# Kernel tuning notes

Hardware: AMD Instinct MI355X
Metric: run time of the kernel (lower is better)

## Reference

```python
import jax, jax.numpy as jnp
import numpy as np

N_NODES = 50000
N_EDGES = 800000
IN_FEAT = 128
HEADS = 8
HEAD_DIM = 16  # out_feat // num_heads = 128 // 8
NEG_SLOPE = 0.2


def setup_inputs() -> dict:
    key = jax.random.key(0)
    ks = jax.random.split(key, 8)
    g = 1.0 / np.sqrt(IN_FEAT)
    return {
        "x": jax.random.normal(ks[0], (N_NODES, IN_FEAT), jnp.float32),
        "efeat": jax.random.normal(ks[1], (N_EDGES, IN_FEAT), jnp.float32),
        "src": jax.random.randint(ks[2], (N_EDGES,), 0, N_NODES),
        "dst": jax.random.randint(ks[3], (N_EDGES,), 0, N_NODES),
        "W_src": jax.random.normal(ks[4], (HEADS * HEAD_DIM, IN_FEAT), jnp.float32) * g,
        "b_src": jnp.zeros((HEADS * HEAD_DIM,), jnp.float32),
        "W_dst": jax.random.normal(ks[5], (HEADS * HEAD_DIM, IN_FEAT), jnp.float32) * g,
        "b_dst": jnp.zeros((HEADS * HEAD_DIM,), jnp.float32),
        "W_edge": jax.random.normal(ks[6], (HEADS * HEAD_DIM, IN_FEAT), jnp.float32) * g,
        "attn": jax.random.normal(ks[7], (HEADS, HEAD_DIM), jnp.float32) * (1.0 / np.sqrt(HEAD_DIM)),
    }


def reference(x, efeat, src, dst, W_src, b_src, W_dst, b_dst, W_edge, attn):
    H, D = HEADS, HEAD_DIM
    # node/edge projections: [N,H,D] / [E,H,D]
    feat_src = (x @ W_src.T + b_src).reshape(-1, H, D)
    feat_dst = (x @ W_dst.T + b_dst).reshape(-1, H, D)
    feat_edge = (efeat @ W_edge.T).reshape(-1, H, D)

    # per-edge GATv2 score: LeakyReLU(src + dst + edge) . attn  -> [E,H]
    fs = feat_src[src]                                    # gather [E,H,D]
    tmp = fs + feat_dst[dst] + feat_edge
    e = jnp.where(tmp >= 0, tmp, NEG_SLOPE * tmp)
    score = jnp.einsum('ehd,hd->eh', e, attn)

    # edge softmax normalized per destination node
    m = jax.ops.segment_max(score, dst, num_segments=N_NODES)     # [N,H]
    ex = jnp.exp(score - jax.lax.stop_gradient(m)[dst])
    z = jax.ops.segment_sum(ex, dst, num_segments=N_NODES)        # [N,H]
    a = ex / z[dst]                                               # [E,H]

    # weighted scatter-sum of (src + edge) messages
    msg = (fs + feat_edge) * a[:, :, None]                        # [E,H,D]
    h = jax.ops.segment_sum(msg, dst, num_segments=N_NODES)       # [N,H,D]

    # res_fc is None since in_feat == H*D; activation = relu
    h = jax.nn.relu(h)
    return h.reshape(N_NODES, H * D)
```

## Files before the change

### kernel.cpp

```cpp
#include <hip/hip_runtime.h>
#include <hip/hip_bf16.h>

#define NNODES 50000
#define NEDGES 800000
#define NEG_SLOPE 0.2f
#define N_PAD 50176

typedef float f32x4 __attribute__((ext_vector_type(4)));
typedef float f32x2 __attribute__((ext_vector_type(2)));
typedef __bf16 bf16x8 __attribute__((ext_vector_type(8)));
typedef __bf16 bf16x4 __attribute__((ext_vector_type(4)));
typedef __bf16 bf16x2 __attribute__((ext_vector_type(2)));

__global__ __launch_bounds__(256) void convert_hist(
    const float* __restrict__ W0, const float* __restrict__ W1,
    const float* __restrict__ W2, __bf16* __restrict__ out,
    const int* __restrict__ dst, int* __restrict__ deg, int* __restrict__ arr)
{
  int b = blockIdx.x;
  if (b < 48) {
    int m = b >> 4;
    const float* W = (m == 0) ? W0 : ((m == 1) ? W1 : W2);
    __bf16* o = out + m * 16384;
    int i = (b & 15) * 1024 + threadIdx.x * 4;
    int r = i >> 7, cx = i & 127;
    f32x4 v = *(const f32x4*)(W + i);
    int kb = cx >> 3, ko = cx & 7;
    int off = r * 128 + ((kb ^ (r & 15)) << 3) + ko;
    bf16x4 pk = { (__bf16)v.x, (__bf16)v.y, (__bf16)v.z, (__bf16)v.w };
    *(bf16x4*)(o + off) = pk;
  } else {
    int e = (b - 48) * 256 + threadIdx.x;
    arr[e] = atomicAdd(&deg[dst[e]], 1);
  }
}

template<int OUT_BF16, int HAS_BIAS, int SCATTER>
__device__ __forceinline__ void gemm_body(
    int tile, const float* __restrict__ A, const __bf16* __restrict__ Wsw,
    const float* __restrict__ bias, const int* __restrict__ rank,
    void* __restrict__ outp, int M, __bf16* sS)
{
  const int t = threadIdx.x;
  const int m0 = tile * 128;

  #pragma unroll
  for (int it = 0; it < 8; ++it) {
    int lin = it * 2048 + t * 8;
    *(bf16x8*)(sS + lin) = *(const bf16x8*)(Wsw + lin);
  }

  const int w = t >> 6, lane = t & 63;
  const int rsel = lane & 15, quad = lane >> 4;

  bf16x8 af[4][2];
  #pragma unroll
  for (int mi = 0; mi < 2; ++mi) {
    int gr = m0 + w * 32 + mi * 16 + rsel;
    const float* p = A + (size_t)gr * 128 + (quad << 3);
    bool ok = gr < M;
    f32x4 r0[4], r1[4];
    #pragma unroll
    for (int kk = 0; kk < 4; ++kk) {
      f32x4 z4 = {0.f, 0.f, 0.f, 0.f};
      r0[kk] = ok ? *(const f32x4*)(p + kk * 32)     : z4;
      r1[kk] = ok ? *(const f32x4*)(p + kk * 32 + 4) : z4;
    }
    #pragma unroll
    for (int kk = 0; kk < 4; ++kk)
      af[kk][mi] = (bf16x8){ (__bf16)r0[kk].x, (__bf16)r0[kk].y, (__bf16)r0[kk].z, (__bf16)r0[kk].w,
                             (__bf16)r1[kk].x, (__bf16)r1[kk].y, (__bf16)r1[kk].z, (__bf16)r1[kk].w };
  }

  f32x4 acc[2][8];
  f32x4 zero = {0.f, 0.f, 0.f, 0.f};
  #pragma unroll
  for (int mi = 0; mi < 2; ++mi)
    #pragma unroll
    for (int ni = 0; ni < 8; ++ni) acc[mi][ni] = zero;

  __syncthreads();

  #pragma unroll
  for (int kk = 0; kk < 4; ++kk) {
    int kb0 = kk * 4 + quad;
    bf16x8 bfr[8];
    #pragma unroll
    for (int ni = 0; ni < 8; ++ni) {
      int r = ni * 16 + rsel;
      bfr[ni] = *(const bf16x8*)(sS + r * 128 + ((kb0 ^ (r & 15)) << 3));
    }
    #pragma unroll
    for (int mi = 0; mi < 2; ++mi)
      #pragma unroll
      for (int ni = 0; ni < 8; ++ni)
        acc[mi][ni] = __builtin_amdgcn_mfma_f32_16x16x32_bf16(af[kk][mi], bfr[ni], acc[mi][ni], 0, 0, 0);
  }

  if (OUT_BF16 && SCATTER) {
    __syncthreads();
    #pragma unroll
    for (int mi = 0; mi < 2; ++mi)
      #pragma unroll
      for (int ni = 0; ni < 8; ++ni)
        #pragma unroll
        for (int r4 = 0; r4 < 4; ++r4) {
          float v = acc[mi][ni][r4];
          float vx = __shfl_xor(v, 1);
          if (!(rsel & 1)) {
            int trow = w * 32 + mi * 16 + quad * 4 + r4;
            bf16x2 pkv = { (__bf16)v, (__bf16)vx };
            *(bf16x2*)(sS + trow * 136 + ni * 16 + rsel) = pkv;
          }
        }
    __syncthreads();
    int tr = t >> 1, h = t & 1;
    int grow = m0 + tr;
    if (grow < M) {
      int orw = rank[grow];
      const __bf16* sp = sS + tr * 136 + h * 64;
      __bf16* dp = (__bf16*)outp + (size_t)orw * 128 + h * 64;
      #pragma unroll
      for (int i = 0; i < 8; ++i)
        *(bf16x8*)(dp + i * 8) = *(const bf16x8*)(sp + i * 8);
    }
  } else {
    #pragma unroll
    for (int mi = 0; mi < 2; ++mi)
      #pragma unroll
      for (int ni = 0; ni < 8; ++ni)
        #pragma unroll
        for (int r4 = 0; r4 < 4; ++r4) {
          int grow = m0 + w * 32 + mi * 16 + quad * 4 + r4;
          int col = ni * 16 + rsel;
          if (grow < M) {
            float v = acc[mi][ni][r4];
            if (HAS_BIAS) v += bias[col];
            ((float*)outp)[(size_t)grow * 128 + col] = v;
          }
        }
  }
}

__global__ __launch_bounds__(256, 4) void proj_all(
    const float* __restrict__ x, const float* __restrict__ efeat,
    const __bf16* __restrict__ wsw, const float* __restrict__ b_src,
    const float* __restrict__ b_dst, const int* __restrict__ rank,
    float* __restrict__ feat_src, float* __restrict__ feat_dst,
    __bf16* __restrict__ fe)
{
  __shared__ __bf16 sS[128 * 136];
  int b = blockIdx.x;
  if (b < 6250)
    gemm_body<1,0,1>(b, efeat, wsw + 32768, nullptr, rank, fe, NEDGES, sS);
  else if (b < 6641)
    gemm_body<0,1,0>(b - 6250, x, wsw, b_src, nullptr, feat_src, NNODES, sS);
  else
    gemm_body<0,1,0>(b - 6641, x, wsw + 16384, b_dst, nullptr, feat_dst, NNODES, sS);
}

__global__ void scan_local(const int* __restrict__ deg, int* __restrict__ scanned,
                           int* __restrict__ bsum){
  __shared__ int s[1024];
  int t = threadIdx.x, i = blockIdx.x * 1024 + t;
  int v = deg[i];
  s[t] = v; __syncthreads();
  #pragma unroll
  for (int off = 1; off < 1024; off <<= 1){
    int x = (t >= off) ? s[t - off] : 0;
    __syncthreads();
    s[t] += x;
    __syncthreads();
  }
  scanned[i] = s[t] - v;
  if (t == 1023) bsum[blockIdx.x] = s[t];
}

__global__ void scan_add(const int* __restrict__ scanned, const int* __restrict__ bsum,
                         int* __restrict__ row_start){
  __shared__ int sbase;
  int b = blockIdx.x, t = threadIdx.x;
  if (t == 0){
    int lim = b >> 2, acc = 0;
    for (int j = 0; j < lim; ++j) acc += bsum[j];
    sbase = acc;
  }
  __syncthreads();
  int i = b * 256 + t;
  if (i < N_PAD) row_start[i] = scanned[i] + sbase;
}

__global__ void scatter_kernel(const int* __restrict__ dst, const int* __restrict__ src,
                               const int* __restrict__ row_start, int* __restrict__ rank,
                               int* __restrict__ src_perm){
  int e = blockIdx.x * 256 + threadIdx.x;
  int pos = row_start[dst[e]] + rank[e];
  rank[e] = pos;
  src_perm[pos] = src[e];
}

__global__ __launch_bounds__(256) void aggregate_fused(
    const int* __restrict__ row_start, const int* __restrict__ deg,
    const int* __restrict__ src_perm, const float* __restrict__ fs,
    const float* __restrict__ fd, const __bf16* __restrict__ fe,
    const float* __restrict__ attn, float* __restrict__ out)
{
  int wv = threadIdx.x >> 6, lane = threadIdx.x & 63;
  int n = blockIdx.x * 4 + wv;
  int row = row_start[n], dg = deg[n];
  int c = lane << 1;
  f32x2 fdv = *(const f32x2*)(fd + (size_t)n * 128 + c);
  f32x2 atv = *(const f32x2*)(attn + c);
  float acc0 = 0.f, acc1 = 0.f, zs = 0.f;
  const __bf16* fep = fe + (size_t)row * 128 + c;

  #define EDGE_BODY(FV, EV)                                            \
    {                                                                  \
      float v0 = (FV).x + (float)(EV).x;                               \
      float v1 = (FV).y + (float)(EV).y;                               \
      float t0 = v0 + fdv.x; t0 = t0 >= 0.f ? t0 : NEG_SLOPE * t0;     \
      float t1 = v1 + fdv.y; t1 = t1 >= 0.f ? t1 : NEG_SLOPE * t1;     \
      float p = t0 * atv.x + t1 * atv.y;                               \
      p += __shfl_xor(p, 1);                                           \
      p += __shfl_xor(p, 2);                                           \
      p += __shfl_xor(p, 4);                                           \
      float ex = __expf(p);                                            \
      acc0 += ex * v0; acc1 += ex * v1; zs += ex;                      \
    }

  for (int base = 0; base < dg; base += 64){
    int cnt = min(64, dg - base);
    int si = 0;
    if (lane < cnt) si = src_perm[row + base + lane];
    int j = 0;
    for (; j + 4 <= cnt; j += 4){
      int s0 = __shfl(si, j,     64);
      int s1 = __shfl(si, j + 1, 64);
      int s2 = __shfl(si, j + 2, 64);
      int s3 = __shfl(si, j + 3, 64);
      f32x2 f0 = *(const f32x2*)(fs + (size_t)s0 * 128 + c);
      f32x2 f1 = *(const f32x2*)(fs + (size_t)s1 * 128 + c);
      f32x2 f2 = *(const f32x2*)(fs + (size_t)s2 * 128 + c);
      f32x2 f3 = *(const f32x2*)(fs + (size_t)s3 * 128 + c);
      bf16x2 e0 = *(const bf16x2*)(fep + (size_t)(base + j)     * 128);
      bf16x2 e1 = *(const bf16x2*)(fep + (size_t)(base + j + 1) * 128);
      bf16x2 e2 = *(const bf16x2*)(fep + (size_t)(base + j + 2) * 128);
      bf16x2 e3 = *(const bf16x2*)(fep + (size_t)(base + j + 3) * 128);
      EDGE_BODY(f0, e0)
      EDGE_BODY(f1, e1)
      EDGE_BODY(f2, e2)
      EDGE_BODY(f3, e3)
    }
    for (; j < cnt; ++j){
      int s0 = __shfl(si, j, 64);
      f32x2 f0 = *(const f32x2*)(fs + (size_t)s0 * 128 + c);
      bf16x2 e0 = *(const bf16x2*)(fep + (size_t)(base + j) * 128);
      EDGE_BODY(f0, e0)
    }
  }
  #undef EDGE_BODY

  float rz = zs > 0.f ? 1.f / zs : 0.f;
  float o0 = acc0 * rz, o1 = acc1 * rz;
  f32x2 ov = { o0 > 0.f ? o0 : 0.f, o1 > 0.f ? o1 : 0.f };
  *(f32x2*)(out + (size_t)n * 128 + c) = ov;
}

extern "C" void kernel_launch(void* const* d_in, const int* in_sizes, int n_in,
                              void* d_out, int out_size, void* d_ws, size_t ws_size,
                              hipStream_t stream)
{
  const float* x      = (const float*)d_in[0];
  const float* efeat  = (const float*)d_in[1];
  const int*   src    = (const int*)d_in[2];
  const int*   dst    = (const int*)d_in[3];
  const float* W_src  = (const float*)d_in[4];
  const float* b_src  = (const float*)d_in[5];
  const float* W_dst  = (const float*)d_in[6];
  const float* b_dst  = (const float*)d_in[7];
  const float* W_edge = (const float*)d_in[8];
  const float* attn   = (const float*)d_in[9];

  char* ws = (char*)d_ws;
  float*  feat_src  = (float*)(ws + 0);
  float*  feat_dst  = (float*)(ws + 25600000);
  __bf16* fe        = (__bf16*)(ws + 51200000);
  int*    src_perm  = (int*)  (ws + 256000000);
  int*    rank      = (int*)  (ws + 259200000);
  int*    row_start = (int*)  (ws + 262400000);
  int*    scanned   = (int*)  (ws + 262801408);
  int*    deg       = (int*)  (ws + 263002112);
  int*    bsum      = (int*)  (ws + 263202816);
  __bf16* wsw       = (__bf16*)(ws + 263203840);

  hipMemsetAsync(deg, 0, 200704, stream);

  convert_hist<<<3173, 256, 0, stream>>>(W_src, W_dst, W_edge, wsw, dst, deg, rank);

  scan_local    <<<49, 1024, 0, stream>>>(deg, scanned, bsum);
  scan_add      <<<196, 256, 0, stream>>>(scanned, bsum, row_start);
  scatter_kernel<<<3125, 256, 0, stream>>>(dst, src, row_start, rank, src_perm);

  proj_all<<<7032, 256, 0, stream>>>(x, efeat, wsw, b_src, b_dst, rank,
                                     feat_src, feat_dst, fe);

  aggregate_fused<<<12500, 256, 0, stream>>>(row_start, deg, src_perm, feat_src,
                                             feat_dst, fe, attn, (float*)d_out);
}
```

Baseline: 770.8 us.

## Move per-edge score and message computation into the edge projection epilogue

The node projection GEMMs are merged into the scan_add kernel launch, and the scatter kernel is removed. The edge GEMM epilogue now gathers the src and dst node features, computes the per-head attention score and its exp, and writes the bf16 message (fs+fe) and the exp values to CSR-sorted positions. Aggregation then becomes a streaming weighted sum over contiguous messages with no random gathers or shuffle reductions. In exchange it writes an extra exp buffer and a bf16 message buffer. Softmax is now computed without subtracting the segment max, which could overflow for large scores.

Result: slower. 909.7 us (+18.0%).

```diff
diff --git a/kernel.cpp b/kernel.cpp
--- a/kernel.cpp
+++ b/kernel.cpp
@@ -35,11 +35,9 @@
   }
 }
 
-template<int OUT_BF16, int HAS_BIAS, int SCATTER>
-__device__ __forceinline__ void gemm_body(
+__device__ __forceinline__ void gemm_node(
     int tile, const float* __restrict__ A, const __bf16* __restrict__ Wsw,
-    const float* __restrict__ bias, const int* __restrict__ rank,
-    void* __restrict__ outp, int M, __bf16* sS)
+    const float* __restrict__ bias, float* __restrict__ outp, int M, __bf16* sS)
 {
   const int t = threadIdx.x;
   const int m0 = tile * 128;
@@ -97,66 +95,17 @@
         acc[mi][ni] = __builtin_amdgcn_mfma_f32_16x16x32_bf16(af[kk][mi], bfr[ni], acc[mi][ni], 0, 0, 0);
   }
 
-  if (OUT_BF16 && SCATTER) {
-    __syncthreads();
-    #pragma unroll
-    for (int mi = 0; mi < 2; ++mi)
-      #pragma unroll
-      for (int ni = 0; ni < 8; ++ni)
-        #pragma unroll
-        for (int r4 = 0; r4 < 4; ++r4) {
-          float v = acc[mi][ni][r4];
-          float vx = __shfl_xor(v, 1);
-          if (!(rsel & 1)) {
-            int trow = w * 32 + mi * 16 + quad * 4 + r4;
-            bf16x2 pkv = { (__bf16)v, (__bf16)vx };
-            *(bf16x2*)(sS + trow * 136 + ni * 16 + rsel) = pkv;
-          }
-        }
-    __syncthreads();
-    int tr = t >> 1, h = t & 1;
-    int grow = m0 + tr;
-    if (grow < M) {
-      int orw = rank[grow];
-      const __bf16* sp = sS + tr * 136 + h * 64;
-      __bf16* dp = (__bf16*)outp + (size_t)orw * 128 + h * 64;
-      #pragma unroll
-      for (int i = 0; i < 8; ++i)
-        *(bf16x8*)(dp + i * 8) = *(const bf16x8*)(sp + i * 8);
-    }
-  } else {
-    #pragma unroll
-    for (int mi = 0; mi < 2; ++mi)
-      #pragma unroll
-      for (int ni = 0; ni < 8; ++ni)
-        #pragma unroll
-        for (int r4 = 0; r4 < 4; ++r4) {
-          int grow = m0 + w * 32 + mi * 16 + quad * 4 + r4;
-          int col = ni * 16 + rsel;
-          if (grow < M) {
-            float v = acc[mi][ni][r4];
-            if (HAS_BIAS) v += bias[col];
-            ((float*)outp)[(size_t)grow * 128 + col] = v;
-          }
-        }
-  }
-}
-
-__global__ __launch_bounds__(256, 4) void proj_all(
-    const float* __restrict__ x, const float* __restrict__ efeat,
-    const __bf16* __restrict__ wsw, const float* __restrict__ b_src,
-    const float* __restrict__ b_dst, const int* __restrict__ rank,
-    float* __restrict__ feat_src, float* __restrict__ feat_dst,
-    __bf16* __restrict__ fe)
-{
-  __shared__ __bf16 sS[128 * 136];
-  int b = blockIdx.x;
-  if (b < 6250)
-    gemm_body<1,0,1>(b, efeat, wsw + 32768, nullptr, rank, fe, NEDGES, sS);
-  else if (b < 6641)
-    gemm_body<0,1,0>(b - 6250, x, wsw, b_src, nullptr, feat_src, NNODES, sS);
-  else
-    gemm_body<0,1,0>(b - 6641, x, wsw + 16384, b_dst, nullptr, feat_dst, NNODES, sS);
+  #pragma unroll
+  for (int mi = 0; mi < 2; ++mi)
+    #pragma unroll
+    for (int ni = 0; ni < 8; ++ni)
+      #pragma unroll
+      for (int r4 = 0; r4 < 4; ++r4) {
+        int grow = m0 + w * 32 + mi * 16 + quad * 4 + r4;
+        int col = ni * 16 + rsel;
+        if (grow < M)
+          outp[(size_t)grow * 128 + col] = acc[mi][ni][r4] + bias[col];
+      }
 }
 
 __global__ void scan_local(const int* __restrict__ deg, int* __restrict__ scanned,
@@ -176,92 +125,188 @@
   if (t == 1023) bsum[blockIdx.x] = s[t];
 }
 
-__global__ void scan_add(const int* __restrict__ scanned, const int* __restrict__ bsum,
-                         int* __restrict__ row_start){
+__global__ __launch_bounds__(256, 4) void scan_nodes(
+    const int* __restrict__ scanned, const int* __restrict__ bsum,
+    int* __restrict__ row_start,
+    const float* __restrict__ x, const __bf16* __restrict__ wsw,
+    const float* __restrict__ b_src, const float* __restrict__ b_dst,
+    float* __restrict__ feat_src, float* __restrict__ feat_dst)
+{
+  __shared__ __bf16 sS[128 * 136];
   __shared__ int sbase;
-  int b = blockIdx.x, t = threadIdx.x;
-  if (t == 0){
-    int lim = b >> 2, acc = 0;
-    for (int j = 0; j < lim; ++j) acc += bsum[j];
-    sbase = acc;
-  }
+  int b = blockIdx.x;
+  if (b < 196) {
+    int t = threadIdx.x;
+    if (t == 0){
+      int lim = b >> 2, a = 0;
+      for (int j = 0; j < lim; ++j) a += bsum[j];
+      sbase = a;
+    }
+    __syncthreads();
+    int i = b * 256 + t;
+    if (i < N_PAD) row_start[i] = scanned[i] + sbase;
+  } else if (b < 587) {
+    gemm_node(b - 196, x, wsw,         b_src, feat_src, NNODES, sS);
+  } else {
+    gemm_node(b - 587, x, wsw + 16384, b_dst, feat_dst, NNODES, sS);
+  }
+}
+
+__global__ __launch_bounds__(256, 4) void proj_edge(
+    const float* __restrict__ efeat, const __bf16* __restrict__ Wsw,
+    const int* __restrict__ src, const int* __restrict__ dst,
+    const int* __restrict__ arr, const int* __restrict__ row_start,
+    const float* __restrict__ fs, const float* __restrict__ fd,
+    const float* __restrict__ attn,
+    __bf16* __restrict__ msg, float* __restrict__ exbuf)
+{
+  __shared__ __bf16 sS[128 * 136];
+  const int t = threadIdx.x;
+  const int m0 = blockIdx.x * 128;
+
+  #pragma unroll
+  for (int it = 0; it < 8; ++it) {
+    int lin = it * 2048 + t * 8;
+    *(bf16x8*)(sS + lin) = *(const bf16x8*)(Wsw + lin);
+  }
+
+  const int w = t >> 6, lane = t & 63;
+  const int rsel = lane & 15, quad = lane >> 4;
+
+  bf16x8 af[4][2];
+  #pragma unroll
+  for (int mi = 0; mi < 2; ++mi) {
+    int gr = m0 + w * 32 + mi * 16 + rsel;
+    const float* p = efeat + (size_t)gr * 128 + (quad << 3);
+    f32x4 r0[4], r1[4];
+    #pragma unroll
+    for (int kk = 0; kk < 4; ++kk) {
+      r0[kk] = *(const f32x4*)(p + kk * 32);
+      r1[kk] = *(const f32x4*)(p + kk * 32 + 4);
+    }
+    #pragma unroll
+    for (int kk = 0; kk < 4; ++kk)
+      af[kk][mi] = (bf16x8){ (__bf16)r0[kk].x, (__bf16)r0[kk].y, (__bf16)r0[kk].z, (__bf16)r0[kk].w,
+                             (__bf16)r1[kk].x, (__bf16)r1[kk].y, (__bf16)r1[kk].z, (__bf16)r1[kk].w };
+  }
+
+  f32x4 acc[2][8];
+  f32x4 zero = {0.f, 0.f, 0.f, 0.f};
+  #pragma unroll
+  for (int mi = 0; mi < 2; ++mi)
+    #pragma unroll
+    for (int ni = 0; ni < 8; ++ni) acc[mi][ni] = zero;
+
   __syncthreads();
-  int i = b * 256 + t;
-  if (i < N_PAD) row_start[i] = scanned[i] + sbase;
-}
-
-__global__ void scatter_kernel(const int* __restrict__ dst, const int* __restrict__ src,
-                               const int* __restrict__ row_start, int* __restrict__ rank,
-                               int* __restrict__ src_perm){
-  int e = blockIdx.x * 256 + threadIdx.x;
-  int pos = row_start[dst[e]] + rank[e];
-  rank[e] = pos;
-  src_perm[pos] = src[e];
-}
-
-__global__ __launch_bounds__(256) void aggregate_fused(
+
+  #pragma unroll
+  for (int kk = 0; kk < 4; ++kk) {
+    int kb0 = kk * 4 + quad;
+    bf16x8 bfr[8];
+    #pragma unroll
+    for (int ni = 0; ni < 8; ++ni) {
+      int r = ni * 16 + rsel;
+      bfr[ni] = *(const bf16x8*)(sS + r * 128 + ((kb0 ^ (r & 15)) << 3));
+    }
+    #pragma unroll
+    for (int mi = 0; mi < 2; ++mi)
+      #pragma unroll
+      for (int ni = 0; ni < 8; ++ni)
+        acc[mi][ni] = __builtin_amdgcn_mfma_f32_16x16x32_bf16(af[kk][mi], bfr[ni], acc[mi][ni], 0, 0, 0);
+  }
+
+  __syncthreads();
+  #pragma unroll
+  for (int mi = 0; mi < 2; ++mi)
+    #pragma unroll
+    for (int ni = 0; ni < 8; ++ni)
+      #pragma unroll
+      for (int r4 = 0; r4 < 4; ++r4) {
+        float v = acc[mi][ni][r4];
+        float vx = __shfl_xor(v, 1);
+        if (!(rsel & 1)) {
+          int trow = w * 32 + mi * 16 + quad * 4 + r4;
+          bf16x2 pkv = { (__bf16)v, (__bf16)vx };
+          *(bf16x2*)(sS + trow * 136 + ni * 16 + rsel) = pkv;
+        }
+      }
+  __syncthreads();
+
+  int tr = t >> 1, h = t & 1;
+  int e = m0 + tr;
+  int d = dst[e], s = src[e];
+  int pos = row_start[d] + arr[e];
+  const float* fsp = fs + (size_t)s * 128 + h * 64;
+  const float* fdp = fd + (size_t)d * 128 + h * 64;
+  const float* atp = attn + h * 64;
+  __bf16* mp = msg + (size_t)pos * 128 + h * 64;
+  float exs[4];
+  #pragma unroll
+  for (int hc = 0; hc < 4; ++hc) {
+    f32x4 fa[4], fb[4], fat[4];
+    #pragma unroll
+    for (int i = 0; i < 4; ++i) {
+      fa[i]  = *(const f32x4*)(fsp + hc * 16 + i * 4);
+      fb[i]  = *(const f32x4*)(fdp + hc * 16 + i * 4);
+      fat[i] = *(const f32x4*)(atp + hc * 16 + i * 4);
+    }
+    union { __bf16 m16[16]; bf16x8 m8[2]; } mu;
+    float sc = 0.f;
+    #pragma unroll
+    for (int i = 0; i < 4; ++i) {
+      bf16x4 fev = *(const bf16x4*)(sS + tr * 136 + h * 64 + hc * 16 + i * 4);
+      #pragma unroll
+      for (int j = 0; j < 4; ++j) {
+        float v = fa[i][j] + (float)fev[j];
+        mu.m16[i * 4 + j] = (__bf16)v;
+        float u = v + fb[i][j];
+        u = u >= 0.f ? u : NEG_SLOPE * u;
+        sc += u * fat[i][j];
+      }
+    }
+    *(bf16x8*)(mp + hc * 16)     = mu.m8[0];
+    *(bf16x8*)(mp + hc * 16 + 8) = mu.m8[1];
+    exs[hc] = __expf(sc);
+  }
+  *(f32x4*)(exbuf + (size_t)pos * 8 + h * 4) = (f32x4){exs[0], exs[1], exs[2], exs[3]};
+}
+
+__global__ __launch_bounds__(256) void aggregate_slim(
     const int* __restrict__ row_start, const int* __restrict__ deg,
-    const int* __restrict__ src_perm, const float* __restrict__ fs,
-    const float* __restrict__ fd, const __bf16* __restrict__ fe,
-    const float* __restrict__ attn, float* __restrict__ out)
+    const __bf16* __restrict__ msg, const float* __restrict__ exbuf,
+    float* __restrict__ out)
 {
   int wv = threadIdx.x >> 6, lane = threadIdx.x & 63;
   int n = blockIdx.x * 4 + wv;
   int row = row_start[n], dg = deg[n];
-  int c = lane << 1;
-  f32x2 fdv = *(const f32x2*)(fd + (size_t)n * 128 + c);
-  f32x2 atv = *(const f32x2*)(attn + c);
-  float acc0 = 0.f, acc1 = 0.f, zs = 0.f;
-  const __bf16* fep = fe + (size_t)row * 128 + c;
-
-  #define EDGE_BODY(FV, EV)                                            \
-    {                                                                  \
-      float v0 = (FV).x + (float)(EV).x;                               \
-      float v1 = (FV).y + (float)(EV).y;                               \
-      float t0 = v0 + fdv.x; t0 = t0 >= 0.f ? t0 : NEG_SLOPE * t0;     \
-      float t1 = v1 + fdv.y; t1 = t1 >= 0.f ? t1 : NEG_SLOPE * t1;     \
-      float p = t0 * atv.x + t1 * atv.y;                               \
-      p += __shfl_xor(p, 1);                                           \
-      p += __shfl_xor(p, 2);                                           \
-      p += __shfl_xor(p, 4);                                           \
-      float ex = __expf(p);                                            \
-      acc0 += ex * v0; acc1 += ex * v1; zs += ex;                      \
-    }
-
-  for (int base = 0; base < dg; base += 64){
-    int cnt = min(64, dg - base);
-    int si = 0;
-    if (lane < cnt) si = src_perm[row + base + lane];
-    int j = 0;
-    for (; j + 4 <= cnt; j += 4){
-      int s0 = __shfl(si, j,     64);
-      int s1 = __shfl(si, j + 1, 64);
-      int s2 = __shfl(si, j + 2, 64);
-      int s3 = __shfl(si, j + 3, 64);
-      f32x2 f0 = *(const f32x2*)(fs + (size_t)s0 * 128 + c);
-      f32x2 f1 = *(const f32x2*)(fs + (size_t)s1 * 128 + c);
-      f32x2 f2 = *(const f32x2*)(fs + (size_t)s2 * 128 + c);
-      f32x2 f3 = *(const f32x2*)(fs + (size_t)s3 * 128 + c);
-      bf16x2 e0 = *(const bf16x2*)(fep + (size_t)(base + j)     * 128);
-      bf16x2 e1 = *(const bf16x2*)(fep + (size_t)(base + j + 1) * 128);
-      bf16x2 e2 = *(const bf16x2*)(fep + (size_t)(base + j + 2) * 128);
-      bf16x2 e3 = *(const bf16x2*)(fep + (size_t)(base + j + 3) * 128);
-      EDGE_BODY(f0, e0)
-      EDGE_BODY(f1, e1)
-      EDGE_BODY(f2, e2)
-      EDGE_BODY(f3, e3)
-    }
-    for (; j < cnt; ++j){
-      int s0 = __shfl(si, j, 64);
-      f32x2 f0 = *(const f32x2*)(fs + (size_t)s0 * 128 + c);
-      bf16x2 e0 = *(const bf16x2*)(fep + (size_t)(base + j) * 128);
-      EDGE_BODY(f0, e0)
-    }
-  }
-  #undef EDGE_BODY
+  int c = lane << 1, hd = lane >> 3;
+  float a0 = 0.f, a1 = 0.f, zs = 0.f;
+  const __bf16* mp = msg + (size_t)row * 128 + c;
+  const float*  ep = exbuf + (size_t)row * 8 + hd;
+
+  int j = 0;
+  for (; j + 4 <= dg; j += 4) {
+    float e0 = ep[(size_t)(j + 0) * 8];
+    float e1 = ep[(size_t)(j + 1) * 8];
+    float e2 = ep[(size_t)(j + 2) * 8];
+    float e3 = ep[(size_t)(j + 3) * 8];
+    bf16x2 m0 = *(const bf16x2*)(mp + (size_t)(j + 0) * 128);
+    bf16x2 m1 = *(const bf16x2*)(mp + (size_t)(j + 1) * 128);
+    bf16x2 m2 = *(const bf16x2*)(mp + (size_t)(j + 2) * 128);
+    bf16x2 m3 = *(const bf16x2*)(mp + (size_t)(j + 3) * 128);
+    a0 += e0 * (float)m0.x; a1 += e0 * (float)m0.y; zs += e0;
+    a0 += e1 * (float)m1.x; a1 += e1 * (float)m1.y; zs += e1;
+    a0 += e2 * (float)m2.x; a1 += e2 * (float)m2.y; zs += e2;
+    a0 += e3 * (float)m3.x; a1 += e3 * (float)m3.y; zs += e3;
+  }
+  for (; j < dg; ++j) {
+    float e0 = ep[(size_t)j * 8];
+    bf16x2 m0 = *(const bf16x2*)(mp + (size_t)j * 128);
+    a0 += e0 * (float)m0.x; a1 += e0 * (float)m0.y; zs += e0;
+  }
 
   float rz = zs > 0.f ? 1.f / zs : 0.f;
-  float o0 = acc0 * rz, o1 = acc1 * rz;
+  float o0 = a0 * rz, o1 = a1 * rz;
   f32x2 ov = { o0 > 0.f ? o0 : 0.f, o1 > 0.f ? o1 : 0.f };
   *(f32x2*)(out + (size_t)n * 128 + c) = ov;
 }
@@ -284,26 +329,26 @@
   char* ws = (char*)d_ws;
   float*  feat_src  = (float*)(ws + 0);
   float*  feat_dst  = (float*)(ws + 25600000);
-  __bf16* fe        = (__bf16*)(ws + 51200000);
-  int*    src_perm  = (int*)  (ws + 256000000);
-  int*    rank      = (int*)  (ws + 259200000);
-  int*    row_start = (int*)  (ws + 262400000);
-  int*    scanned   = (int*)  (ws + 262801408);
-  int*    deg       = (int*)  (ws + 263002112);
-  int*    bsum      = (int*)  (ws + 263202816);
-  __bf16* wsw       = (__bf16*)(ws + 263203840);
+  __bf16* msg       = (__bf16*)(ws + 51200000);
+  float*  exbuf     = (float*)(ws + 256000000);
+  int*    arr       = (int*)  (ws + 281600000);
+  int*    row_start = (int*)  (ws + 284800000);
+  int*    scanned   = (int*)  (ws + 285000704);
+  int*    deg       = (int*)  (ws + 285201408);
+  int*    bsum      = (int*)  (ws + 285402112);
+  __bf16* wsw       = (__bf16*)(ws + 285403136);
 
   hipMemsetAsync(deg, 0, 200704, stream);
 
-  convert_hist<<<3173, 256, 0, stream>>>(W_src, W_dst, W_edge, wsw, dst, deg, rank);
-
-  scan_local    <<<49, 1024, 0, stream>>>(deg, scanned, bsum);
-  scan_add      <<<196, 256, 0, stream>>>(scanned, bsum, row_start);
-  scatter_kernel<<<3125, 256, 0, stream>>>(dst, src, row_start, rank, src_perm);
-
-  proj_all<<<7032, 256, 0, stream>>>(x, efeat, wsw, b_src, b_dst, rank,
-                                     feat_src, feat_dst, fe);
-
-  aggregate_fused<<<12500, 256, 0, stream>>>(row_start, deg, src_perm, feat_src,
-                                             feat_dst, fe, attn, (float*)d_out);
-}
+  convert_hist<<<3173, 256, 0, stream>>>(W_src, W_dst, W_edge, wsw, dst, deg, arr);
+
+  scan_local<<<49, 1024, 0, stream>>>(deg, scanned, bsum);
+
+  scan_nodes<<<978, 256, 0, stream>>>(scanned, bsum, row_start, x, wsw,
+                                      b_src, b_dst, feat_src, feat_dst);
+
+  proj_edge<<<6250, 256, 0, stream>>>(efeat, wsw + 32768, src, dst, arr, row_start,
+                                      feat_src, feat_dst, attn, msg, exbuf);
+
+  aggregate_slim<<<12500, 256, 0, stream>>>(row_start, deg, msg, exbuf, (float*)d_out);
+}
```

## Fuse CSR scatter into edge projection GEMM and deepen aggregate gather unroll

Applied to the files above, without the earlier changes.

Removes the separate scatter kernel: the edge-projection GEMM now computes each edge's CSR position from row_start and the atomic arrival index, and writes both src_perm and the bf16 edge features there. It also restructures the aggregation inner loop to issue 8 independent gathers before computing, instead of 4. This saves a kernel launch and a pass over the edge arrays, and exposes more memory-level parallelism in the gather loop. The cost is more registers in the aggregate loop and extra index loads inside the GEMM epilogue.

New measurement: 815.0 us. 5.7% more time.

```diff
diff --git a/kernel.cpp b/kernel.cpp
--- a/kernel.cpp
+++ b/kernel.cpp
@@ -35,15 +35,42 @@
   }
 }
 
-template<int OUT_BF16, int HAS_BIAS, int SCATTER>
-__device__ __forceinline__ void gemm_body(
-    int tile, const float* __restrict__ A, const __bf16* __restrict__ Wsw,
-    const float* __restrict__ bias, const int* __restrict__ rank,
-    void* __restrict__ outp, int M, __bf16* sS)
+__global__ void scan_local(const int* __restrict__ deg, int* __restrict__ scanned,
+                           int* __restrict__ bsum){
+  __shared__ int s[1024];
+  int t = threadIdx.x, i = blockIdx.x * 1024 + t;
+  int v = deg[i];
+  s[t] = v; __syncthreads();
+  #pragma unroll
+  for (int off = 1; off < 1024; off <<= 1){
+    int x = (t >= off) ? s[t - off] : 0;
+    __syncthreads();
+    s[t] += x;
+    __syncthreads();
+  }
+  scanned[i] = s[t] - v;
+  if (t == 1023) bsum[blockIdx.x] = s[t];
+}
+
+__global__ void scan_add(const int* __restrict__ scanned, const int* __restrict__ bsum,
+                         int* __restrict__ row_start){
+  __shared__ int sbase;
+  int b = blockIdx.x, t = threadIdx.x;
+  if (t == 0){
+    int lim = b >> 2, acc = 0;
+    for (int j = 0; j < lim; ++j) acc += bsum[j];
+    sbase = acc;
+  }
+  __syncthreads();
+  int i = b * 256 + t;
+  if (i < N_PAD) row_start[i] = scanned[i] + sbase;
+}
+
+__device__ __forceinline__ void gemm_core(
+    int m0, const float* __restrict__ A, const __bf16* __restrict__ Wsw,
+    int M, __bf16* sS, f32x4 (&acc)[2][8])
 {
   const int t = threadIdx.x;
-  const int m0 = tile * 128;
-
   #pragma unroll
   for (int it = 0; it < 8; ++it) {
     int lin = it * 2048 + t * 8;
@@ -72,7 +99,6 @@
                              (__bf16)r1[kk].x, (__bf16)r1[kk].y, (__bf16)r1[kk].z, (__bf16)r1[kk].w };
   }
 
-  f32x4 acc[2][8];
   f32x4 zero = {0.f, 0.f, 0.f, 0.f};
   #pragma unroll
   for (int mi = 0; mi < 2; ++mi)
@@ -96,8 +122,29 @@
       for (int ni = 0; ni < 8; ++ni)
         acc[mi][ni] = __builtin_amdgcn_mfma_f32_16x16x32_bf16(af[kk][mi], bfr[ni], acc[mi][ni], 0, 0, 0);
   }
-
-  if (OUT_BF16 && SCATTER) {
+}
+
+__global__ __launch_bounds__(256, 4) void proj_all(
+    const float* __restrict__ x, const float* __restrict__ efeat,
+    const __bf16* __restrict__ wsw, const float* __restrict__ b_src,
+    const float* __restrict__ b_dst,
+    const int* __restrict__ src, const int* __restrict__ dst,
+    const int* __restrict__ arr, const int* __restrict__ row_start,
+    float* __restrict__ feat_src, float* __restrict__ feat_dst,
+    __bf16* __restrict__ fe, int* __restrict__ src_perm)
+{
+  __shared__ __bf16 sS[128 * 136];
+  int b = blockIdx.x;
+  const int t = threadIdx.x;
+  f32x4 acc[2][8];
+
+  if (b < 6250) {
+    int m0 = b * 128;
+    gemm_core(m0, efeat, wsw + 32768, NEDGES, sS, acc);
+
+    const int w = t >> 6, lane = t & 63;
+    const int rsel = lane & 15, quad = lane >> 4;
+
     __syncthreads();
     #pragma unroll
     for (int mi = 0; mi < 2; ++mi)
@@ -115,16 +162,24 @@
         }
     __syncthreads();
     int tr = t >> 1, h = t & 1;
-    int grow = m0 + tr;
-    if (grow < M) {
-      int orw = rank[grow];
-      const __bf16* sp = sS + tr * 136 + h * 64;
-      __bf16* dp = (__bf16*)outp + (size_t)orw * 128 + h * 64;
-      #pragma unroll
-      for (int i = 0; i < 8; ++i)
-        *(bf16x8*)(dp + i * 8) = *(const bf16x8*)(sp + i * 8);
-    }
+    int e = m0 + tr;
+    int pos = row_start[dst[e]] + arr[e];
+    if (h == 0) src_perm[pos] = src[e];
+    const __bf16* sp = sS + tr * 136 + h * 64;
+    __bf16* dp = fe + (size_t)pos * 128 + h * 64;
+    #pragma unroll
+    for (int i = 0; i < 8; ++i)
+      *(bf16x8*)(dp + i * 8) = *(const bf16x8*)(sp + i * 8);
   } else {
+    const float* bias;
+    float* outp;
+    int m0;
+    if (b < 6641) { m0 = (b - 6250) * 128; bias = b_src; outp = feat_src; }
+    else          { m0 = (b - 6641) * 128; bias = b_dst; outp = feat_dst; }
+    gemm_core(m0, x, b < 6641 ? wsw : wsw + 16384, NNODES, sS, acc);
+
+    const int w = t >> 6, lane = t & 63;
+    const int rsel = lane & 15, quad = lane >> 4;
     #pragma unroll
     for (int mi = 0; mi < 2; ++mi)
       #pragma unroll
@@ -133,70 +188,10 @@
         for (int r4 = 0; r4 < 4; ++r4) {
           int grow = m0 + w * 32 + mi * 16 + quad * 4 + r4;
           int col = ni * 16 + rsel;
-          if (grow < M) {
-            float v = acc[mi][ni][r4];
-            if (HAS_BIAS) v += bias[col];
-            ((float*)outp)[(size_t)grow * 128 + col] = v;
-          }
+          if (grow < NNODES)
+            outp[(size_t)grow * 128 + col] = acc[mi][ni][r4] + bias[col];
         }
   }
-}
-
-__global__ __launch_bounds__(256, 4) void proj_all(
-    const float* __restrict__ x, const float* __restrict__ efeat,
-    const __bf16* __restrict__ wsw, const float* __restrict__ b_src,
-    const float* __restrict__ b_dst, const int* __restrict__ rank,
-    float* __restrict__ feat_src, float* __restrict__ feat_dst,
-    __bf16* __restrict__ fe)
-{
-  __shared__ __bf16 sS[128 * 136];
-  int b = blockIdx.x;
-  if (b < 6250)
-    gemm_body<1,0,1>(b, efeat, wsw + 32768, nullptr, rank, fe, NEDGES, sS);
-  else if (b < 6641)
-    gemm_body<0,1,0>(b - 6250, x, wsw, b_src, nullptr, feat_src, NNODES, sS);
-  else
-    gemm_body<0,1,0>(b - 6641, x, wsw + 16384, b_dst, nullptr, feat_dst, NNODES, sS);
-}
-
-__global__ void scan_local(const int* __restrict__ deg, int* __restrict__ scanned,
-                           int* __restrict__ bsum){
-  __shared__ int s[1024];
-  int t = threadIdx.x, i = blockIdx.x * 1024 + t;
-  int v = deg[i];
-  s[t] = v; __syncthreads();
-  #pragma unroll
-  for (int off = 1; off < 1024; off <<= 1){
-    int x = (t >= off) ? s[t - off] : 0;
-    __syncthreads();
-    s[t] += x;
-    __syncthreads();
-  }
-  scanned[i] = s[t] - v;
-  if (t == 1023) bsum[blockIdx.x] = s[t];
-}
-
-__global__ void scan_add(const int* __restrict__ scanned, const int* __restrict__ bsum,
-                         int* __restrict__ row_start){
-  __shared__ int sbase;
-  int b = blockIdx.x, t = threadIdx.x;
-  if (t == 0){
-    int lim = b >> 2, acc = 0;
-    for (int j = 0; j < lim; ++j) acc += bsum[j];
-    sbase = acc;
-  }
-  __syncthreads();
-  int i = b * 256 + t;
-  if (i < N_PAD) row_start[i] = scanned[i] + sbase;
-}
-
-__global__ void scatter_kernel(const int* __restrict__ dst, const int* __restrict__ src,
-                               const int* __restrict__ row_start, int* __restrict__ rank,
-                               int* __restrict__ src_perm){
-  int e = blockIdx.x * 256 + threadIdx.x;
-  int pos = row_start[dst[e]] + rank[e];
-  rank[e] = pos;
-  src_perm[pos] = src[e];
 }
 
 __global__ __launch_bounds__(256) void aggregate_fused(
@@ -233,23 +228,18 @@
     int si = 0;
     if (lane < cnt) si = src_perm[row + base + lane];
     int j = 0;
-    for (; j + 4 <= cnt; j += 4){
-      int s0 = __shfl(si, j,     64);
-      int s1 = __shfl(si, j + 1, 64);
-      int s2 = __shfl(si, j + 2, 64);
-      int s3 = __shfl(si, j + 3, 64);
-      f32x2 f0 = *(const f32x2*)(fs + (size_t)s0 * 128 + c);
-      f32x2 f1 = *(const f32x2*)(fs + (size_t)s1 * 128 + c);
-      f32x2 f2 = *(const f32x2*)(fs + (size_t)s2 * 128 + c);
-      f32x2 f3 = *(const f32x2*)(fs + (size_t)s3 * 128 + c);
-      bf16x2 e0 = *(const bf16x2*)(fep + (size_t)(base + j)     * 128);
-      bf16x2 e1 = *(const bf16x2*)(fep + (size_t)(base + j + 1) * 128);
-      bf16x2 e2 = *(const bf16x2*)(fep + (size_t)(base + j + 2) * 128);
-      bf16x2 e3 = *(const bf16x2*)(fep + (size_t)(base + j + 3) * 128);
-      EDGE_BODY(f0, e0)
-      EDGE_BODY(f1, e1)
-      EDGE_BODY(f2, e2)
-      EDGE_BODY(f3, e3)
+    for (; j + 8 <= cnt; j += 8){
+      int sx[8];
+      f32x2 fx[8];
+      bf16x2 ex[8];
+      #pragma unroll
+      for (int u = 0; u < 8; ++u) sx[u] = __shfl(si, j + u, 64);
+      #pragma unroll
+      for (int u = 0; u < 8; ++u) fx[u] = *(const f32x2*)(fs + (size_t)sx[u] * 128 + c);
+      #pragma unroll
+      for (int u = 0; u < 8; ++u) ex[u] = *(const bf16x2*)(fep + (size_t)(base + j + u) * 128);
+      #pragma unroll
+      for (int u = 0; u < 8; ++u) EDGE_BODY(fx[u], ex[u])
     }
     for (; j < cnt; ++j){
       int s0 = __shfl(si, j, 64);
@@ -286,23 +276,23 @@
   float*  feat_dst  = (float*)(ws + 25600000);
   __bf16* fe        = (__bf16*)(ws + 51200000);
   int*    src_perm  = (int*)  (ws + 256000000);
-  int*    rank      = (int*)  (ws + 259200000);
+  int*    arr       = (int*)  (ws + 259200000);
   int*    row_start = (int*)  (ws + 262400000);
-  int*    scanned   = (int*)  (ws + 262801408);
-  int*    deg       = (int*)  (ws + 263002112);
-  int*    bsum      = (int*)  (ws + 263202816);
-  __bf16* wsw       = (__bf16*)(ws + 263203840);
+  int*    scanned   = (int*)  (ws + 262601408);
+  int*    deg       = (int*)  (ws + 262802112);
+  int*    bsum      = (int*)  (ws + 263002816);
+  __bf16* wsw       = (__bf16*)(ws + 263003840);
 
   hipMemsetAsync(deg, 0, 200704, stream);
 
-  convert_hist<<<3173, 256, 0, stream>>>(W_src, W_dst, W_edge, wsw, dst, deg, rank);
-
-  scan_local    <<<49, 1024, 0, stream>>>(deg, scanned, bsum);
-  scan_add      <<<196, 256, 0, stream>>>(scanned, bsum, row_start);
-  scatter_kernel<<<3125, 256, 0, stream>>>(dst, src, row_start, rank, src_perm);
-
-  proj_all<<<7032, 256, 0, stream>>>(x, efeat, wsw, b_src, b_dst, rank,
-                                     feat_src, feat_dst, fe);
+  convert_hist<<<3173, 256, 0, stream>>>(W_src, W_dst, W_edge, wsw, dst, deg, arr);
+
+  scan_local<<<49, 1024, 0, stream>>>(deg, scanned, bsum);
+  scan_add  <<<196, 256, 0, stream>>>(scanned, bsum, row_start);
+
+  proj_all<<<7032, 256, 0, stream>>>(x, efeat, wsw, b_src, b_dst,
+                                     src, dst, arr, row_start,
+                                     feat_src, feat_dst, fe, src_perm);
 
   aggregate_fused<<<12500, 256, 0, stream>>>(row_start, deg, src_perm, feat_src,
                                              feat_dst, fe, attn, (float*)d_out);
```
